# Performance work log

Measured on AMD Instinct MI355X. Metric: run time of the kernel, lower is better.

## Reference

```python
import jax, jax.numpy as jnp
import numpy as np

L_LAYERS = 2
SEQ = 2048
K_EIG = 24
D = 128
D_TGT = 64
K_U = 3
K_Y = 2
B = 8


def hankel_eigh(n, k):
    # Z[i,j] = 2 / ((i+j)^3 - (i+j)), 1-indexed; top-k eigenpairs
    s = np.arange(1, n + 1, dtype=np.float64)
    ij = s[:, None] + s[None, :]
    z = 2.0 / (ij ** 3 - ij)
    vals, vecs = np.linalg.eigh(z)
    return (jnp.asarray(vals[-k:], jnp.float32), jnp.asarray(vecs[:, -k:], jnp.float32))


def setup_inputs() -> dict:
    key = jax.random.key(0)
    ks = jax.random.split(key, 8)
    sd = 1.0 / np.sqrt(D)
    inp = {
        "x": jax.random.normal(ks[0], (B, SEQ, D), jnp.float32),
        "emb_w": jax.random.normal(ks[1], (D, D), jnp.float32) * sd,
        "emb_b": jnp.zeros((D,), jnp.float32),
        "ln_g": jnp.ones((L_LAYERS, D), jnp.float32),
        "ln_b": jnp.zeros((L_LAYERS, D), jnp.float32),
        "m_phi": jax.random.normal(ks[2], (L_LAYERS, K_EIG * D, D), jnp.float32) * sd,
        "m_u": jax.random.normal(ks[3], (L_LAYERS, D, D, K_U), jnp.float32) * sd,
        "m_y": jax.random.normal(ks[4], (L_LAYERS, D, K_Y, D), jnp.float32) * 0.01,
        "w1": jax.random.normal(ks[5], (L_LAYERS, D, 2 * D), jnp.float32) * sd,
        "b1": jnp.zeros((L_LAYERS, 2 * D), jnp.float32),
        "proj_w": jax.random.normal(ks[6], (D, D_TGT), jnp.float32) * sd,
        "proj_b": jnp.zeros((D_TGT,), jnp.float32),
    }
    ev, evec = hankel_eigh(SEQ, K_EIG)
    inp["eig_vals"] = ev
    inp["eig_vecs"] = evec
    return inp


def compute_x_tilde(x, eig_vals, eig_vecs):
    # x: [B, L, D]; causal (truncated full) convolution of each eigvec filter
    # with each input channel via FFT. Result [B, L, K, D] -> [B, L, K*D].
    n = 2 * SEQ
    V = jnp.fft.rfft(eig_vecs, n=n, axis=0)              # [nf, K]
    U = jnp.fft.rfft(x, n=n, axis=1)                     # [B, nf, D]
    conv = jnp.fft.irfft(V[None, :, :, None] * U[:, :, None, :], n=n, axis=1)[:, :SEQ]
    conv = conv * (eig_vals ** 0.25)[None, None, :, None]
    return conv.reshape(x.shape[0], SEQ, K_EIG * x.shape[-1]).astype(x.dtype)


def compute_ar_x_preds(m_u, x):
    # o[t] = sum_{i<K_U} m_u[:, :, i] @ x[t-i]  (zero for t-i < 0)
    res = jnp.einsum('bli,oi->blo', x, m_u[:, :, 0])
    for i in range(1, K_U):
        xi = jnp.pad(x, ((0, 0), (i, 0), (0, 0)))[:, :SEQ]
        res = res + jnp.einsum('bli,oi->blo', xi, m_u[:, :, i])
    return res


def compute_y_t(m_y, deltas):
    # y[t] = sum_{j<K_Y} m_y[:, j, :] @ y[t-1-j] + deltas[t]
    d = deltas.shape[-1]
    def step(carry, x):  # carry [B, K_Y, d] holds y[t-1], y[t-2], ...
        out = jnp.einsum('okd,bkd->bo', m_y, carry) + x
        carry = jnp.concatenate([out[:, None, :], carry[:, :-1]], axis=1)
        return carry, out
    init = jnp.zeros((deltas.shape[0], K_Y, d), deltas.dtype)
    _, ys = jax.lax.scan(step, init, jnp.swapaxes(deltas, 0, 1))
    return jnp.swapaxes(ys, 0, 1)


def layer_norm(x, g, b):
    mu = x.mean(-1, keepdims=True)
    var = ((x - mu) ** 2).mean(-1, keepdims=True)
    return (x - mu) / jnp.sqrt(var + 1e-5) * g + b


def reference(x, emb_w, emb_b, ln_g, ln_b, m_phi, m_u, m_y, w1, b1, proj_w, proj_b, eig_vals, eig_vecs):
    h = x @ emb_w + emb_b
    for i in range(L_LAYERS):
        z = h
        h = layer_norm(h, ln_g[i], ln_b[i])
        x_tilde = compute_x_tilde(h, eig_vals, eig_vecs)       # [B, L, K*D]
        delta = x_tilde @ m_phi[i] + compute_ar_x_preds(m_u[i], h)
        y = compute_y_t(m_y[i], delta)
        y = jax.nn.gelu(y, approximate=False)
        y = y @ w1[i] + b1[i]
        a, g = jnp.split(y, 2, axis=-1)
        h = a * jax.nn.sigmoid(g) + z                          # GLU + residual (dropout=0)
    return h @ proj_w + proj_b
```

## Files before the change

### kernel.cpp

```cpp
#include <hip/hip_runtime.h>

typedef unsigned short u16;
typedef unsigned int u32;
typedef __bf16 bf16x8 __attribute__((ext_vector_type(8)));
typedef float f32x4 __attribute__((ext_vector_type(4)));
typedef float f32x2 __attribute__((ext_vector_type(2)));
typedef u16 u16x4 __attribute__((ext_vector_type(4)));
typedef u16 u16x8 __attribute__((ext_vector_type(8)));

#define DEV static __device__ __forceinline__

static constexpr int ROWS = 8 * 2048;
static constexpr int TAPS = 24;
static constexpr int PADR = 64;
static constexpr int DROWS = 2048 + PADR;

DEV u16 f2bf(float x) {
  u32 u = __float_as_uint(x);
  u += 0x7fffu + ((u >> 16) & 1u);
  return (u16)(u >> 16);
}

DEV void gld_lds16(const u16* g, u16* l) {
  __builtin_amdgcn_global_load_lds(
      (const __attribute__((address_space(1))) u32*)g,
      (__attribute__((address_space(3))) u32*)l, 16, 0, 0);
}


__global__ void prep_toeplitz(const float* __restrict__ evec,
                              const float* __restrict__ evals,
                              u16* __restrict__ T) {
  int k = blockIdx.x / 33, ti = blockIdx.x % 33;
  float sc = powf(evals[k], 0.25f);
  u16* out = T + (size_t)blockIdx.x * 4096;
  for (int e = threadIdx.x; e < 4096; e += 256) {
    int i = e >> 6, j = e & 63;
    int tau = (ti - 1) * 64 + i - j;
    float v = (tau >= 0 && tau < 2048) ? evec[tau * 24 + k] * sc : 0.f;
    out[e] = f2bf(v);
  }
}

__global__ void transpose_w(const float* __restrict__ src, u16* __restrict__ dst,
                            int K, int N) {
  int idx = blockIdx.x * 256 + threadIdx.x;
  if (idx >= K * N) return;
  int n = idx / K, k = idx % K;
  dst[idx] = f2bf(src[(size_t)k * N + n]);
}

__global__ void prep_mphiT(const float* __restrict__ mphi,
                           const float* __restrict__ mu,
                           u16* __restrict__ dst) {
  int idx = blockIdx.x * 256 + threadIdx.x;
  if (idx >= 128 * 3456) return;
  int o = idx / 3456, c = idx % 3456;
  float v;
  if (c < 3072) {
    v = mphi[(size_t)c * 128 + o];
  } else {
    int cc = c - 3072;
    int j = cc >> 7, i = cc & 127;
    v = mu[((size_t)o * 128 + i) * 3 + j];
  }
  dst[idx] = f2bf(v);
}

__global__ void f32_to_bf16_k(const float* __restrict__ src, u16* __restrict__ dst,
                              int n4) {
  int i = blockIdx.x * 256 + threadIdx.x;
  if (i >= n4) return;
  f32x4 v = *(const f32x4*)(src + (size_t)i * 4);
  u16x4 o;
  o[0] = f2bf(v[0]); o[1] = f2bf(v[1]); o[2] = f2bf(v[2]); o[3] = f2bf(v[3]);
  *(u16x4*)(dst + (size_t)i * 4) = o;
}

__global__ __launch_bounds__(128) void hprep_kernel(const float* __restrict__ my,
                                                    u16* __restrict__ Hp) {
  const int l = blockIdx.x >> 7, j = blockIdx.x & 127;
  const int o = threadIdx.x;
  const float* M = my + (size_t)l * 32768;
  u32 mp1[64], mp2[64];
  {
    const float* r1 = M + (size_t)o * 256;
    const float* r2 = r1 + 128;
#pragma unroll
    for (int q = 0; q < 64; ++q) {
      mp1[q] = (u32)f2bf(r1[2 * q]) | ((u32)f2bf(r1[2 * q + 1]) << 16);
      mp2[q] = (u32)f2bf(r2[2 * q]) | ((u32)f2bf(r2[2 * q + 1]) << 16);
    }
  }
  __shared__ float vb[3][128];
  u16* HpL = Hp + ((size_t)l * 128 + o) * (TAPS * 128) + j;
  float v0 = (o == j) ? 1.f : 0.f;
  vb[0][o] = v0;
  vb[2][o] = 0.f;
  HpL[0] = f2bf(v0);
  __syncthreads();
  for (int tau = 1; tau < TAPS; ++tau) {
    const int a = (tau + 2) % 3;
    const int b = (tau + 1) % 3;
    const int c = tau % 3;
    const float* v1 = vb[a];
    const float* v2 = vb[b];
    float acc = 0.f;
#pragma unroll
    for (int q = 0; q < 64; ++q) {
      u32 w1 = mp1[q], w2 = mp2[q];
      float m1lo = __uint_as_float(w1 << 16);
      float m1hi = __uint_as_float(w1 & 0xffff0000u);
      float m2lo = __uint_as_float(w2 << 16);
      float m2hi = __uint_as_float(w2 & 0xffff0000u);
      acc += m1lo * v1[2 * q] + m1hi * v1[2 * q + 1];
      acc += m2lo * v2[2 * q] + m2hi * v2[2 * q + 1];
    }
    vb[c][o] = acc;
    HpL[tau * 128] = f2bf(acc);
    __syncthreads();
  }
}

__global__ void zero_pad(u16* __restrict__ dpad) {
  int i = blockIdx.x * 256 + threadIdx.x;
  int b = i >> 10, off = i & 1023;
  *(u16x8*)(dpad + (size_t)b * DROWS * 128 + off * 8) = (u16x8){0, 0, 0, 0, 0, 0, 0, 0};
}


__global__ __launch_bounds__(256) void ln_kernel(
    const float* __restrict__ h, const float* __restrict__ gam,
    const float* __restrict__ bet, u16* __restrict__ out) {
  int row = blockIdx.x * 4 + (threadIdx.x >> 6);
  int lane = threadIdx.x & 63;
  f32x2 v = *(const f32x2*)(h + (size_t)row * 128 + lane * 2);
  float s = v[0] + v[1];
#pragma unroll
  for (int o = 32; o; o >>= 1) s += __shfl_xor(s, o);
  float mu = s * (1.f / 128.f);
  float dx = v[0] - mu, dy = v[1] - mu;
  float q = dx * dx + dy * dy;
#pragma unroll
  for (int o = 32; o; o >>= 1) q += __shfl_xor(q, o);
  float rstd = rsqrtf(q * (1.f / 128.f) + 1e-5f);
  f32x2 g2 = *(const f32x2*)(gam + lane * 2);
  f32x2 b2 = *(const f32x2*)(bet + lane * 2);
  float o0 = dx * rstd * g2[0] + b2[0];
  float o1 = dy * rstd * g2[1] + b2[1];
  u32 pk = (u32)f2bf(o0) | ((u32)f2bf(o1) << 16);
  *(u32*)(out + (size_t)row * 128 + lane * 2) = pk;
}

__global__ __launch_bounds__(256) void transpose_hln(
    const u16* __restrict__ src, u16* __restrict__ dst) {
  __shared__ u16 tile[64][72];
  int blk = blockIdx.x;
  int b = blk >> 6, rem = blk & 63;
  int st = rem >> 1, dt = rem & 1;
  int r = threadIdx.x >> 2, cseg = (threadIdx.x & 3) << 4;
  const u16* s = src + ((size_t)(b * 2048 + st * 64 + r)) * 128 + dt * 64 + cseg;
  u16x8 v0 = *(const u16x8*)s;
  u16x8 v1 = *(const u16x8*)(s + 8);
#pragma unroll
  for (int i = 0; i < 8; ++i) tile[r][cseg + i] = v0[i];
#pragma unroll
  for (int i = 0; i < 8; ++i) tile[r][cseg + 8 + i] = v1[i];
  __syncthreads();
  int dr = threadIdx.x >> 2, sseg = (threadIdx.x & 3) << 4;
  u16x8 w0, w1;
#pragma unroll
  for (int i = 0; i < 8; ++i) w0[i] = tile[sseg + i][dr];
#pragma unroll
  for (int i = 0; i < 8; ++i) w1[i] = tile[sseg + 8 + i][dr];
  u16* d = dst + ((size_t)(b * 128 + dt * 64 + dr)) * 2048 + st * 64 + sseg;
  *(u16x8*)d = w0;
  *(u16x8*)(d + 8) = w1;
}

__global__ void shift_kernel(const u16* __restrict__ hln, u16* __restrict__ xtc) {
  int row = blockIdx.x;
  int t = row & 2047;
  int d = threadIdx.x;
#pragma unroll
  for (int j = 0; j < 3; ++j) {
    u16 v = (t >= j) ? hln[(size_t)(row - j) * 128 + d] : (u16)0;
    xtc[(size_t)row * 3456 + 3072 + j * 128 + d] = v;
  }
}

__global__ void glu_kernel(const float* __restrict__ y2, float* __restrict__ h,
                           u16* __restrict__ hbf, int n4) {
  int i = blockIdx.x * 256 + threadIdx.x;
  if (i >= n4) return;
  int row = i >> 5, d4 = i & 31;
  f32x4 a = *(const f32x4*)(y2 + (size_t)row * 256 + d4 * 4);
  f32x4 g = *(const f32x4*)(y2 + (size_t)row * 256 + 128 + d4 * 4);
  f32x4 hv = *(const f32x4*)(h + (size_t)i * 4);
  f32x4 hn;
  u16x4 o;
#pragma unroll
  for (int j = 0; j < 4; ++j) {
    hn[j] = a[j] * (1.f / (1.f + expf(-g[j]))) + hv[j];
    o[j] = f2bf(hn[j]);
  }
  *(f32x4*)(h + (size_t)i * 4) = hn;
  *(u16x4*)(hbf + (size_t)i * 4) = o;
}


template <int BM, int BN>
__global__ __launch_bounds__(256) void gemm_bt(
    const u16* __restrict__ A, int lda, const u16* __restrict__ BT, int ldbt,
    float* __restrict__ C, int ldc, const float* __restrict__ bias, int kBlocks,
    int accumulate, u16* __restrict__ Cbf) {
  constexpr int WROWS = (BN == 64) ? 4 : 2;
  constexpr int WCOLS = (BN == 64) ? 1 : 2;
  constexpr int WTM = BM / WROWS;
  constexpr int WTN = BN / WCOLS;
  constexpr int FM = WTM / 16;
  constexpr int FN = WTN / 16;
  __shared__ u16 As[BM * 64];
  __shared__ u16 Bs[BN * 64];
  const int tid = threadIdx.x;
  const int wid = tid >> 6, lane = tid & 63;
  const int bm = blockIdx.x, bn = blockIdx.y;
  const int wr = wid / WCOLS, wc = wid % WCOLS;
  const int r = lane & 15, hi = lane >> 4;

  f32x4 acc[FM][FN];
#pragma unroll
  for (int i = 0; i < FM; ++i)
#pragma unroll
    for (int j = 0; j < FN; ++j) acc[i][j] = (f32x4){0.f, 0.f, 0.f, 0.f};

  for (int kb = 0; kb < kBlocks; ++kb) {
    if (kb) __syncthreads();
#pragma unroll
    for (int it = 0; it < BM / 32; ++it) {
      int ci = it * 256 + tid;
      int sc = (ci & 7) ^ ((ci >> 3) & 7);
      gld_lds16(A + (size_t)(bm * BM + (ci >> 3)) * lda + kb * 64 + sc * 8,
                &As[(it * 256 + wid * 64) * 8]);
    }
#pragma unroll
    for (int it = 0; it < BN / 32; ++it) {
      int ci = it * 256 + tid;
      int sc = (ci & 7) ^ ((ci >> 3) & 7);
      gld_lds16(BT + (size_t)(bn * BN + (ci >> 3)) * ldbt + kb * 64 + sc * 8,
                &Bs[(it * 256 + wid * 64) * 8]);
    }
    __syncthreads();
#pragma unroll
    for (int ks = 0; ks < 2; ++ks) {
      const int sk = ((ks * 4 + hi) ^ (r & 7)) << 3;
      bf16x8 af[FM], bfv[FN];
#pragma unroll
      for (int fm = 0; fm < FM; ++fm)
        af[fm] = *(const bf16x8*)&As[(wr * WTM + fm * 16 + r) * 64 + sk];
#pragma unroll
      for (int fn = 0; fn < FN; ++fn)
        bfv[fn] = *(const bf16x8*)&Bs[(wc * WTN + fn * 16 + r) * 64 + sk];
#pragma unroll
      for (int fm = 0; fm < FM; ++fm)
#pragma unroll
        for (int fn = 0; fn < FN; ++fn)
          acc[fm][fn] = __builtin_amdgcn_mfma_f32_16x16x32_bf16(
              af[fm], bfv[fn], acc[fm][fn], 0, 0, 0);
    }
  }
#pragma unroll
  for (int fm = 0; fm < FM; ++fm) {
#pragma unroll
    for (int fn = 0; fn < FN; ++fn) {
      const int col = bn * BN + wc * WTN + fn * 16 + r;
      const float bv = bias ? bias[col] : 0.f;
#pragma unroll
      for (int q = 0; q < 4; ++q) {
        const int row = bm * BM + wr * WTM + fm * 16 + hi * 4 + q;
        float v = acc[fm][fn][q] + bv;
        if (C) {
          float* cp = &C[(size_t)row * ldc + col];
          if (accumulate) v += *cp;
          *cp = v;
        }
        if (Cbf) {
          int bb = row >> 11, t = row & 2047;
          Cbf[((size_t)(bb * DROWS + PADR + t)) * 128 + col] = f2bf(v);
        }
      }
    }
  }
}

__global__ __launch_bounds__(256) void gemm_conv(
    const u16* __restrict__ T, const u16* __restrict__ hlnT,
    u16* __restrict__ xtc) {
  __shared__ u16 As[128 * 64];
  __shared__ u16 Bs[128 * 64];
  const int tid = threadIdx.x;
  const int wid = tid >> 6, lane = tid & 63;
  const int tt = blockIdx.x / 192;
  const int rem = blockIdx.x % 192;
  const int kc = rem >> 3, b = rem & 7;
  const int t0 = (15 - tt) << 7;
  const int r = lane & 15, hi = lane >> 4;
  const int wr = wid >> 1, wc = wid & 1;

  f32x4 acc[4][4];
#pragma unroll
  for (int i = 0; i < 4; ++i)
#pragma unroll
    for (int j = 0; j < 4; ++j) acc[i][j] = (f32x4){0.f, 0.f, 0.f, 0.f};

  const u16* Tk = T + (size_t)kc * 33 * 4096;
  const u16* Bb = hlnT + (size_t)b * 128 * 2048;
  const int nsb = (t0 >> 6) + 2;

  for (int sb = 0; sb < nsb; ++sb) {
    const int dlt = (t0 >> 6) - sb;
    if (sb) __syncthreads();
#pragma unroll
    for (int it = 0; it < 4; ++it) {
      int ci = it * 256 + tid;
      int ti = (ci < 512) ? (dlt + 1) : (dlt + 2);
      int lc = ci & 511;
      int sc = (lc & 7) ^ ((lc >> 3) & 7);
      gld_lds16(Tk + (size_t)ti * 4096 + (lc >> 3) * 64 + sc * 8,
                &As[(it * 256 + wid * 64) * 8]);
    }
#pragma unroll
    for (int it = 0; it < 4; ++it) {
      int ci = it * 256 + tid;
      int sc = (ci & 7) ^ ((ci >> 3) & 7);
      gld_lds16(Bb + (size_t)(ci >> 3) * 2048 + sb * 64 + sc * 8,
                &Bs[(it * 256 + wid * 64) * 8]);
    }
    __syncthreads();
#pragma unroll
    for (int ks = 0; ks < 2; ++ks) {
      const int sk = ((ks * 4 + hi) ^ (r & 7)) << 3;
      bf16x8 af[4], bfv[4];
#pragma unroll
      for (int fm = 0; fm < 4; ++fm)
        af[fm] = *(const bf16x8*)&As[(wr * 64 + fm * 16 + r) * 64 + sk];
#pragma unroll
      for (int fn = 0; fn < 4; ++fn)
        bfv[fn] = *(const bf16x8*)&Bs[(wc * 64 + fn * 16 + r) * 64 + sk];
#pragma unroll
      for (int fm = 0; fm < 4; ++fm)
#pragma unroll
        for (int fn = 0; fn < 4; ++fn)
          acc[fm][fn] = __builtin_amdgcn_mfma_f32_16x16x32_bf16(
              af[fm], bfv[fn], acc[fm][fn], 0, 0, 0);
    }
  }
#pragma unroll
  for (int fm = 0; fm < 4; ++fm) {
#pragma unroll
    for (int fn = 0; fn < 4; ++fn) {
      const int col = wc * 64 + fn * 16 + r;
#pragma unroll
      for (int q = 0; q < 4; ++q) {
        const int row = t0 + wr * 64 + fm * 16 + hi * 4 + q;
        xtc[((size_t)(b * 2048 + row)) * 3456 + kc * 128 + col] = f2bf(acc[fm][fn][q]);
      }
    }
  }
}

__global__ __launch_bounds__(256) void gemm_yconv(
    const u16* __restrict__ dpad, const u16* __restrict__ Hp,
    u16* __restrict__ ybf) {
  __shared__ u16 As[64 * 64];
  __shared__ u16 Bs[64 * 64];
  const int tid = threadIdx.x;
  const int wid = tid >> 6, lane = tid & 63;
  const int bm = blockIdx.x, bn = blockIdx.y;
  const int b = bm >> 5, t0 = (bm & 31) << 6;
  const int r = lane & 15, hi = lane >> 4;

  f32x4 acc[4];
#pragma unroll
  for (int j = 0; j < 4; ++j) acc[j] = (f32x4){0.f, 0.f, 0.f, 0.f};

  const u16* Ab = dpad + (size_t)b * DROWS * 128;
  for (int kb = 0; kb < TAPS * 2; ++kb) {
    const int tap = kb >> 1, i0 = (kb & 1) << 6;
    const u16* Ap = Ab + (size_t)(PADR + t0 - tap) * 128 + i0;
    if (kb) __syncthreads();
#pragma unroll
    for (int it = 0; it < 2; ++it) {
      int ci = it * 256 + tid;
      int sc = (ci & 7) ^ ((ci >> 3) & 7);
      gld_lds16(Ap + (size_t)(ci >> 3) * 128 + sc * 8,
                &As[(it * 256 + wid * 64) * 8]);
    }
#pragma unroll
    for (int it = 0; it < 2; ++it) {
      int ci = it * 256 + tid;
      int sc = (ci & 7) ^ ((ci >> 3) & 7);
      gld_lds16(Hp + (size_t)(bn * 64 + (ci >> 3)) * (TAPS * 128) + kb * 64 + sc * 8,
                &Bs[(it * 256 + wid * 64) * 8]);
    }
    __syncthreads();
#pragma unroll
    for (int ks = 0; ks < 2; ++ks) {
      const int sk = ((ks * 4 + hi) ^ (r & 7)) << 3;
      bf16x8 af = *(const bf16x8*)&As[(wid * 16 + r) * 64 + sk];
      bf16x8 bfv[4];
#pragma unroll
      for (int fn = 0; fn < 4; ++fn)
        bfv[fn] = *(const bf16x8*)&Bs[(fn * 16 + r) * 64 + sk];
#pragma unroll
      for (int fn = 0; fn < 4; ++fn)
        acc[fn] = __builtin_amdgcn_mfma_f32_16x16x32_bf16(af, bfv[fn], acc[fn], 0, 0, 0);
    }
  }
#pragma unroll
  for (int fn = 0; fn < 4; ++fn) {
    const int col = bn * 64 + fn * 16 + r;
#pragma unroll
    for (int q = 0; q < 4; ++q) {
      const int row = t0 + wid * 16 + hi * 4 + q;
      float v = acc[fn][q];
      float gl = 0.5f * v * (1.f + erff(v * 0.70710678118654752f));
      ybf[((size_t)(b * 2048 + row)) * 128 + col] = f2bf(gl);
    }
  }
}


extern "C" void kernel_launch(void* const* d_in, const int* in_sizes, int n_in,
                              void* d_out, int out_size, void* d_ws, size_t ws_size,
                              hipStream_t stream) {
  (void)in_sizes; (void)n_in; (void)out_size; (void)ws_size;
  const float* x = (const float*)d_in[0];
  const float* emb_w = (const float*)d_in[1];
  const float* emb_b = (const float*)d_in[2];
  const float* ln_g = (const float*)d_in[3];
  const float* ln_b = (const float*)d_in[4];
  const float* m_phi = (const float*)d_in[5];
  const float* m_u = (const float*)d_in[6];
  const float* m_y = (const float*)d_in[7];
  const float* w1 = (const float*)d_in[8];
  const float* b1 = (const float*)d_in[9];
  const float* proj_w = (const float*)d_in[10];
  const float* proj_b = (const float*)d_in[11];
  const float* evals = (const float*)d_in[12];
  const float* evec = (const float*)d_in[13];
  float* out = (float*)d_out;

  char* p = (char*)d_ws;
  auto carve = [&](size_t bytes) {
    char* r = p;
    p += (bytes + 255) & ~(size_t)255;
    return r;
  };
  u16* Tbuf = (u16*)carve((size_t)24 * 33 * 4096 * 2);
  u16* embT = (u16*)carve(128 * 128 * 2);
  u16* w1T = (u16*)carve((size_t)2 * 256 * 128 * 2);
  u16* projT = (u16*)carve(64 * 128 * 2);
  u16* mphiT = (u16*)carve((size_t)2 * 128 * 3456 * 2);
  u16* Hp = (u16*)carve((size_t)2 * 128 * TAPS * 128 * 2);
  u16* xbf = (u16*)carve((size_t)ROWS * 128 * 2);
  float* h = (float*)carve((size_t)ROWS * 128 * 4);
  u16* hbf = (u16*)carve((size_t)ROWS * 128 * 2);
  u16* hlnbf = (u16*)carve((size_t)ROWS * 128 * 2);
  u16* hlnT = (u16*)carve((size_t)ROWS * 128 * 2);
  u16* xtc = (u16*)carve((size_t)ROWS * 3456 * 2);
  u16* dpad = (u16*)carve((size_t)8 * DROWS * 128 * 2);
  u16* ybf = (u16*)carve((size_t)ROWS * 128 * 2);
  float* y2 = (float*)carve((size_t)ROWS * 256 * 4);

  prep_toeplitz<<<dim3(24 * 33), dim3(256), 0, stream>>>(evec, evals, Tbuf);
  hprep_kernel<<<dim3(256), dim3(128), 0, stream>>>(m_y, Hp);
  zero_pad<<<dim3(32), dim3(256), 0, stream>>>(dpad);
  transpose_w<<<dim3(64), dim3(256), 0, stream>>>(emb_w, embT, 128, 128);
  transpose_w<<<dim3(128), dim3(256), 0, stream>>>(w1, w1T, 128, 256);
  transpose_w<<<dim3(128), dim3(256), 0, stream>>>(w1 + 128 * 256, w1T + 256 * 128, 128, 256);
  transpose_w<<<dim3(32), dim3(256), 0, stream>>>(proj_w, projT, 128, 64);
  prep_mphiT<<<dim3(1728), dim3(256), 0, stream>>>(m_phi, m_u, mphiT);
  prep_mphiT<<<dim3(1728), dim3(256), 0, stream>>>(
      m_phi + (size_t)3072 * 128, m_u + (size_t)128 * 128 * 3, mphiT + (size_t)128 * 3456);
  f32_to_bf16_k<<<dim3(2048), dim3(256), 0, stream>>>(x, xbf, ROWS * 128 / 4);

  gemm_bt<64, 128><<<dim3(256, 1), dim3(256), 0, stream>>>(
      xbf, 128, embT, 128, h, 128, emb_b, 2, 0, nullptr);

  for (int l = 0; l < 2; ++l) {
    ln_kernel<<<dim3(4096), dim3(256), 0, stream>>>(h, ln_g + l * 128, ln_b + l * 128, hlnbf);
    transpose_hln<<<dim3(512), dim3(256), 0, stream>>>(hlnbf, hlnT);
    shift_kernel<<<dim3(16384), dim3(128), 0, stream>>>(hlnbf, xtc);
    const u16* mT = mphiT + (size_t)l * 128 * 3456;
    gemm_conv<<<dim3(3072), dim3(256), 0, stream>>>(Tbuf, hlnT, xtc);
    gemm_bt<64, 64><<<dim3(256, 2), dim3(256), 0, stream>>>(
        xtc, 3456, mT, 3456, nullptr, 0, nullptr, 54, 0, dpad);
    gemm_yconv<<<dim3(256, 2), dim3(256), 0, stream>>>(
        dpad, Hp + (size_t)l * 128 * TAPS * 128, ybf);
    gemm_bt<64, 128><<<dim3(256, 2), dim3(256), 0, stream>>>(
        ybf, 128, w1T + (size_t)l * 256 * 128, 128, y2, 256, b1 + l * 256, 2, 0, nullptr);
    glu_kernel<<<dim3(2048), dim3(256), 0, stream>>>(y2, h, hbf, ROWS * 32);
  }

  gemm_bt<128, 64><<<dim3(128, 1), dim3(256), 0, stream>>>(
      hbf, 128, projT, 128, out, 64, proj_b, 2, 0, nullptr);
}
```

Before: 507.2 us.

## Fuse spectral conv with m_phi projection, LN with transpose, and w1 GEMM with GLU

The separate Toeplitz conv GEMM that wrote a large bf16 x_tilde buffer, followed by a big K=3456 projection GEMM, is replaced by a fused kernel. Each block convolves four eigen-filters, stages each result in LDS and immediately multiplies it by the matching m_phi slice. Partial sums go to seven fp32 slots (six filter groups plus the AR shift GEMM) and a reduce kernel sums them into the padded delta buffer. LayerNorm and the transpose are merged into one kernel, and the w1 GEMM is fused with the GLU and residual, so the y2 round trip disappears. The cost is extra fp32 partial-buffer traffic and a reduction pass, re-rounding of the conv output to bf16 per filter, and lower occupancy from the larger LDS footprint.

```diff
diff --git a/kernel.cpp b/kernel.cpp
--- a/kernel.cpp
+++ b/kernel.cpp
@@ -14,6 +14,7 @@
 static constexpr int TAPS = 24;
 static constexpr int PADR = 64;
 static constexpr int DROWS = 2048 + PADR;
+static constexpr size_t PSLOT = (size_t)ROWS * 128;
 
 DEV u16 f2bf(float x) {
   u32 u = __float_as_uint(x);
@@ -129,91 +130,78 @@
 }
 
 
-__global__ __launch_bounds__(256) void ln_kernel(
+__global__ __launch_bounds__(256) void ln_tr_kernel(
     const float* __restrict__ h, const float* __restrict__ gam,
-    const float* __restrict__ bet, u16* __restrict__ out) {
-  int row = blockIdx.x * 4 + (threadIdx.x >> 6);
-  int lane = threadIdx.x & 63;
-  f32x2 v = *(const f32x2*)(h + (size_t)row * 128 + lane * 2);
-  float s = v[0] + v[1];
-#pragma unroll
-  for (int o = 32; o; o >>= 1) s += __shfl_xor(s, o);
-  float mu = s * (1.f / 128.f);
-  float dx = v[0] - mu, dy = v[1] - mu;
-  float q = dx * dx + dy * dy;
-#pragma unroll
-  for (int o = 32; o; o >>= 1) q += __shfl_xor(q, o);
-  float rstd = rsqrtf(q * (1.f / 128.f) + 1e-5f);
+    const float* __restrict__ bet, u16* __restrict__ hlnbf,
+    u16* __restrict__ hlnT) {
+  __shared__ u16 tile[64][136];
+  const int b = blockIdx.x >> 5, st = blockIdx.x & 31;
+  const int wrow = threadIdx.x >> 6;
+  const int lane = threadIdx.x & 63;
   f32x2 g2 = *(const f32x2*)(gam + lane * 2);
   f32x2 b2 = *(const f32x2*)(bet + lane * 2);
-  float o0 = dx * rstd * g2[0] + b2[0];
-  float o1 = dy * rstd * g2[1] + b2[1];
-  u32 pk = (u32)f2bf(o0) | ((u32)f2bf(o1) << 16);
-  *(u32*)(out + (size_t)row * 128 + lane * 2) = pk;
-}
-
-__global__ __launch_bounds__(256) void transpose_hln(
-    const u16* __restrict__ src, u16* __restrict__ dst) {
-  __shared__ u16 tile[64][72];
-  int blk = blockIdx.x;
-  int b = blk >> 6, rem = blk & 63;
-  int st = rem >> 1, dt = rem & 1;
-  int r = threadIdx.x >> 2, cseg = (threadIdx.x & 3) << 4;
-  const u16* s = src + ((size_t)(b * 2048 + st * 64 + r)) * 128 + dt * 64 + cseg;
-  u16x8 v0 = *(const u16x8*)s;
-  u16x8 v1 = *(const u16x8*)(s + 8);
-#pragma unroll
-  for (int i = 0; i < 8; ++i) tile[r][cseg + i] = v0[i];
-#pragma unroll
-  for (int i = 0; i < 8; ++i) tile[r][cseg + 8 + i] = v1[i];
+#pragma unroll 4
+  for (int it = 0; it < 16; ++it) {
+    int lr = it * 4 + wrow;
+    size_t row = (size_t)b * 2048 + st * 64 + lr;
+    f32x2 v = *(const f32x2*)(h + row * 128 + lane * 2);
+    float s = v[0] + v[1];
+#pragma unroll
+    for (int o = 32; o; o >>= 1) s += __shfl_xor(s, o);
+    float mu = s * (1.f / 128.f);
+    float dx = v[0] - mu, dy = v[1] - mu;
+    float q = dx * dx + dy * dy;
+#pragma unroll
+    for (int o = 32; o; o >>= 1) q += __shfl_xor(q, o);
+    float rstd = rsqrtf(q * (1.f / 128.f) + 1e-5f);
+    float o0 = dx * rstd * g2[0] + b2[0];
+    float o1 = dy * rstd * g2[1] + b2[1];
+    u32 pk = (u32)f2bf(o0) | ((u32)f2bf(o1) << 16);
+    *(u32*)(hlnbf + row * 128 + lane * 2) = pk;
+    *(u32*)&tile[lr][lane * 2] = pk;
+  }
   __syncthreads();
-  int dr = threadIdx.x >> 2, sseg = (threadIdx.x & 3) << 4;
-  u16x8 w0, w1;
-#pragma unroll
-  for (int i = 0; i < 8; ++i) w0[i] = tile[sseg + i][dr];
-#pragma unroll
-  for (int i = 0; i < 8; ++i) w1[i] = tile[sseg + 8 + i][dr];
-  u16* d = dst + ((size_t)(b * 128 + dt * 64 + dr)) * 2048 + st * 64 + sseg;
-  *(u16x8*)d = w0;
-  *(u16x8*)(d + 8) = w1;
-}
-
-__global__ void shift_kernel(const u16* __restrict__ hln, u16* __restrict__ xtc) {
+  const int d = threadIdx.x >> 1;
+  const int half = threadIdx.x & 1;
+#pragma unroll
+  for (int i = 0; i < 4; ++i) {
+    int sg = half * 4 + i;
+    u16x8 w;
+#pragma unroll
+    for (int j = 0; j < 8; ++j) w[j] = tile[sg * 8 + j][d];
+    *(u16x8*)(hlnT + ((size_t)b * 128 + d) * 2048 + st * 64 + sg * 8) = w;
+  }
+}
+
+__global__ void shift_kernel(const u16* __restrict__ hln, u16* __restrict__ out) {
   int row = blockIdx.x;
   int t = row & 2047;
   int d = threadIdx.x;
 #pragma unroll
   for (int j = 0; j < 3; ++j) {
     u16 v = (t >= j) ? hln[(size_t)(row - j) * 128 + d] : (u16)0;
-    xtc[(size_t)row * 3456 + 3072 + j * 128 + d] = v;
-  }
-}
-
-__global__ void glu_kernel(const float* __restrict__ y2, float* __restrict__ h,
-                           u16* __restrict__ hbf, int n4) {
+    out[(size_t)row * 384 + j * 128 + d] = v;
+  }
+}
+
+__global__ void reduce_kernel(const float* __restrict__ parts,
+                              u16* __restrict__ dpad) {
   int i = blockIdx.x * 256 + threadIdx.x;
-  if (i >= n4) return;
+  f32x4 s = *(const f32x4*)(parts + (size_t)i * 4);
+#pragma unroll
+  for (int g = 1; g < 7; ++g) s += *(const f32x4*)(parts + g * PSLOT + (size_t)i * 4);
   int row = i >> 5, d4 = i & 31;
-  f32x4 a = *(const f32x4*)(y2 + (size_t)row * 256 + d4 * 4);
-  f32x4 g = *(const f32x4*)(y2 + (size_t)row * 256 + 128 + d4 * 4);
-  f32x4 hv = *(const f32x4*)(h + (size_t)i * 4);
-  f32x4 hn;
+  int b = row >> 11, t = row & 2047;
   u16x4 o;
-#pragma unroll
-  for (int j = 0; j < 4; ++j) {
-    hn[j] = a[j] * (1.f / (1.f + expf(-g[j]))) + hv[j];
-    o[j] = f2bf(hn[j]);
-  }
-  *(f32x4*)(h + (size_t)i * 4) = hn;
-  *(u16x4*)(hbf + (size_t)i * 4) = o;
+  o[0] = f2bf(s[0]); o[1] = f2bf(s[1]); o[2] = f2bf(s[2]); o[3] = f2bf(s[3]);
+  *(u16x4*)(dpad + ((size_t)(b * DROWS + PADR + t)) * 128 + d4 * 4) = o;
 }
 
 
 template <int BM, int BN>
 __global__ __launch_bounds__(256) void gemm_bt(
     const u16* __restrict__ A, int lda, const u16* __restrict__ BT, int ldbt,
-    float* __restrict__ C, int ldc, const float* __restrict__ bias, int kBlocks,
-    int accumulate, u16* __restrict__ Cbf) {
+    float* __restrict__ C, int ldc, const float* __restrict__ bias, int kBlocks) {
   constexpr int WROWS = (BN == 64) ? 4 : 2;
   constexpr int WCOLS = (BN == 64) ? 1 : 2;
   constexpr int WTM = BM / WROWS;
@@ -278,95 +266,137 @@
 #pragma unroll
       for (int q = 0; q < 4; ++q) {
         const int row = bm * BM + wr * WTM + fm * 16 + hi * 4 + q;
-        float v = acc[fm][fn][q] + bv;
-        if (C) {
-          float* cp = &C[(size_t)row * ldc + col];
-          if (accumulate) v += *cp;
-          *cp = v;
-        }
-        if (Cbf) {
-          int bb = row >> 11, t = row & 2047;
-          Cbf[((size_t)(bb * DROWS + PADR + t)) * 128 + col] = f2bf(v);
-        }
-      }
-    }
-  }
-}
-
-__global__ __launch_bounds__(256) void gemm_conv(
+        C[(size_t)row * ldc + col] = acc[fm][fn][q] + bv;
+      }
+    }
+  }
+}
+
+__global__ __launch_bounds__(256) void gemm_convd(
     const u16* __restrict__ T, const u16* __restrict__ hlnT,
-    u16* __restrict__ xtc) {
-  __shared__ u16 As[128 * 64];
+    const u16* __restrict__ mphiT, float* __restrict__ parts) {
+  __shared__ u16 As[64 * 64];
   __shared__ u16 Bs[128 * 64];
+  __shared__ u16 Ps[64 * 128];
   const int tid = threadIdx.x;
   const int wid = tid >> 6, lane = tid & 63;
-  const int tt = blockIdx.x / 192;
-  const int rem = blockIdx.x % 192;
-  const int kc = rem >> 3, b = rem & 7;
-  const int t0 = (15 - tt) << 7;
+  const int tt = blockIdx.x / 48;
+  const int rem = blockIdx.x % 48;
+  const int g = rem >> 3, b = rem & 7;
+  const int t0 = (31 - tt) << 6;
+  const int nsb = (t0 >> 6) + 1;
+  const int wr = wid >> 1, wc = wid & 1;
   const int r = lane & 15, hi = lane >> 4;
-  const int wr = wid >> 1, wc = wid & 1;
-
-  f32x4 acc[4][4];
-#pragma unroll
-  for (int i = 0; i < 4; ++i)
-#pragma unroll
-    for (int j = 0; j < 4; ++j) acc[i][j] = (f32x4){0.f, 0.f, 0.f, 0.f};
-
-  const u16* Tk = T + (size_t)kc * 33 * 4096;
+
+  f32x4 accd[2][4];
+#pragma unroll
+  for (int i = 0; i < 2; ++i)
+#pragma unroll
+    for (int j = 0; j < 4; ++j) accd[i][j] = (f32x4){0.f, 0.f, 0.f, 0.f};
+
   const u16* Bb = hlnT + (size_t)b * 128 * 2048;
-  const int nsb = (t0 >> 6) + 2;
-
-  for (int sb = 0; sb < nsb; ++sb) {
-    const int dlt = (t0 >> 6) - sb;
-    if (sb) __syncthreads();
-#pragma unroll
-    for (int it = 0; it < 4; ++it) {
-      int ci = it * 256 + tid;
-      int ti = (ci < 512) ? (dlt + 1) : (dlt + 2);
-      int lc = ci & 511;
-      int sc = (lc & 7) ^ ((lc >> 3) & 7);
-      gld_lds16(Tk + (size_t)ti * 4096 + (lc >> 3) * 64 + sc * 8,
-                &As[(it * 256 + wid * 64) * 8]);
-    }
-#pragma unroll
-    for (int it = 0; it < 4; ++it) {
-      int ci = it * 256 + tid;
-      int sc = (ci & 7) ^ ((ci >> 3) & 7);
-      gld_lds16(Bb + (size_t)(ci >> 3) * 2048 + sb * 64 + sc * 8,
-                &Bs[(it * 256 + wid * 64) * 8]);
-    }
-    __syncthreads();
-#pragma unroll
-    for (int ks = 0; ks < 2; ++ks) {
-      const int sk = ((ks * 4 + hi) ^ (r & 7)) << 3;
-      bf16x8 af[4], bfv[4];
-#pragma unroll
-      for (int fm = 0; fm < 4; ++fm)
-        af[fm] = *(const bf16x8*)&As[(wr * 64 + fm * 16 + r) * 64 + sk];
-#pragma unroll
-      for (int fn = 0; fn < 4; ++fn)
-        bfv[fn] = *(const bf16x8*)&Bs[(wc * 64 + fn * 16 + r) * 64 + sk];
-#pragma unroll
-      for (int fm = 0; fm < 4; ++fm)
+
+  for (int f = 0; f < 4; ++f) {
+    const int k = g * 4 + f;
+    const u16* Tk = T + (size_t)k * 33 * 4096;
+    f32x4 accc[2][4];
+#pragma unroll
+    for (int i = 0; i < 2; ++i)
+#pragma unroll
+      for (int j = 0; j < 4; ++j) accc[i][j] = (f32x4){0.f, 0.f, 0.f, 0.f};
+
+    for (int sb = 0; sb < nsb; ++sb) {
+      const int ti = (t0 >> 6) - sb + 1;
+      __syncthreads();
+#pragma unroll
+      for (int it = 0; it < 2; ++it) {
+        int ci = it * 256 + tid;
+        int sc = (ci & 7) ^ ((ci >> 3) & 7);
+        gld_lds16(Tk + (size_t)ti * 4096 + (ci >> 3) * 64 + sc * 8,
+                  &As[(it * 256 + wid * 64) * 8]);
+      }
+#pragma unroll
+      for (int it = 0; it < 4; ++it) {
+        int ci = it * 256 + tid;
+        int sc = (ci & 7) ^ ((ci >> 3) & 7);
+        gld_lds16(Bb + (size_t)(ci >> 3) * 2048 + sb * 64 + sc * 8,
+                  &Bs[(it * 256 + wid * 64) * 8]);
+      }
+      __syncthreads();
+#pragma unroll
+      for (int ks = 0; ks < 2; ++ks) {
+        const int sk = ((ks * 4 + hi) ^ (r & 7)) << 3;
+        bf16x8 af[2], bfv[4];
+#pragma unroll
+        for (int fm = 0; fm < 2; ++fm)
+          af[fm] = *(const bf16x8*)&As[(wr * 32 + fm * 16 + r) * 64 + sk];
 #pragma unroll
         for (int fn = 0; fn < 4; ++fn)
-          acc[fm][fn] = __builtin_amdgcn_mfma_f32_16x16x32_bf16(
-              af[fm], bfv[fn], acc[fm][fn], 0, 0, 0);
-    }
-  }
-#pragma unroll
-  for (int fm = 0; fm < 4; ++fm) {
+          bfv[fn] = *(const bf16x8*)&Bs[(wc * 64 + fn * 16 + r) * 64 + sk];
+#pragma unroll
+        for (int fm = 0; fm < 2; ++fm)
+#pragma unroll
+          for (int fn = 0; fn < 4; ++fn)
+            accc[fm][fn] = __builtin_amdgcn_mfma_f32_16x16x32_bf16(
+                af[fm], bfv[fn], accc[fm][fn], 0, 0, 0);
+      }
+    }
+#pragma unroll
+    for (int fm = 0; fm < 2; ++fm)
+#pragma unroll
+      for (int fn = 0; fn < 4; ++fn) {
+        const int pcol = wc * 64 + fn * 16 + r;
+        const int c = pcol >> 3;
+#pragma unroll
+        for (int q = 0; q < 4; ++q) {
+          const int prow = wr * 32 + fm * 16 + hi * 4 + q;
+          Ps[prow * 128 + ((c ^ (prow & 7)) << 3) + (pcol & 7)] =
+              f2bf(accc[fm][fn][q]);
+        }
+      }
+#pragma unroll
+    for (int dh = 0; dh < 2; ++dh) {
+      __syncthreads();
+#pragma unroll
+      for (int it = 0; it < 4; ++it) {
+        int ci = it * 256 + tid;
+        int sc = (ci & 7) ^ ((ci >> 3) & 7);
+        gld_lds16(mphiT + (size_t)(ci >> 3) * 3456 + k * 128 + dh * 64 + sc * 8,
+                  &Bs[(it * 256 + wid * 64) * 8]);
+      }
+      __syncthreads();
+#pragma unroll
+      for (int ks = 0; ks < 2; ++ks) {
+        const int sk2 = ((dh * 8 + ks * 4 + hi) ^ (r & 7)) << 3;
+        const int sk = ((ks * 4 + hi) ^ (r & 7)) << 3;
+        bf16x8 pa[2], bfv[4];
+#pragma unroll
+        for (int fm = 0; fm < 2; ++fm)
+          pa[fm] = *(const bf16x8*)&Ps[(wr * 32 + fm * 16 + r) * 128 + sk2];
+#pragma unroll
+        for (int fn = 0; fn < 4; ++fn)
+          bfv[fn] = *(const bf16x8*)&Bs[(wc * 64 + fn * 16 + r) * 64 + sk];
+#pragma unroll
+        for (int fm = 0; fm < 2; ++fm)
+#pragma unroll
+          for (int fn = 0; fn < 4; ++fn)
+            accd[fm][fn] = __builtin_amdgcn_mfma_f32_16x16x32_bf16(
+                pa[fm], bfv[fn], accd[fm][fn], 0, 0, 0);
+      }
+    }
+  }
+  float* P = parts + g * PSLOT + ((size_t)b * 2048) * 128;
+#pragma unroll
+  for (int fm = 0; fm < 2; ++fm)
 #pragma unroll
     for (int fn = 0; fn < 4; ++fn) {
       const int col = wc * 64 + fn * 16 + r;
 #pragma unroll
       for (int q = 0; q < 4; ++q) {
-        const int row = t0 + wr * 64 + fm * 16 + hi * 4 + q;
-        xtc[((size_t)(b * 2048 + row)) * 3456 + kc * 128 + col] = f2bf(acc[fm][fn][q]);
-      }
-    }
-  }
+        const int row = t0 + wr * 32 + fm * 16 + hi * 4 + q;
+        P[(size_t)row * 128 + col] = accd[fm][fn][q];
+      }
+    }
 }
 
 __global__ __launch_bounds__(256) void gemm_yconv(
@@ -427,6 +457,97 @@
       float gl = 0.5f * v * (1.f + erff(v * 0.70710678118654752f));
       ybf[((size_t)(b * 2048 + row)) * 128 + col] = f2bf(gl);
     }
+  }
+}
+
+__global__ __launch_bounds__(256) void gemm_w1glu(
+    const u16* __restrict__ ybf, const u16* __restrict__ w1T,
+    const float* __restrict__ b1, float* __restrict__ h,
+    u16* __restrict__ hbf) {
+  __shared__ u16 As[64 * 64];
+  __shared__ u16 Bs[256 * 64];
+  __shared__ float sg[64][128];
+  const int tid = threadIdx.x;
+  const int wid = tid >> 6, lane = tid & 63;
+  const int bm = blockIdx.x;
+  const int wr = wid >> 1, wc = wid & 1;
+  const int r = lane & 15, hi = lane >> 4;
+
+  f32x4 acc[2][8];
+#pragma unroll
+  for (int i = 0; i < 2; ++i)
+#pragma unroll
+    for (int j = 0; j < 8; ++j) acc[i][j] = (f32x4){0.f, 0.f, 0.f, 0.f};
+
+  for (int kb = 0; kb < 2; ++kb) {
+    if (kb) __syncthreads();
+#pragma unroll
+    for (int it = 0; it < 2; ++it) {
+      int ci = it * 256 + tid;
+      int sc = (ci & 7) ^ ((ci >> 3) & 7);
+      gld_lds16(ybf + (size_t)(bm * 64 + (ci >> 3)) * 128 + kb * 64 + sc * 8,
+                &As[(it * 256 + wid * 64) * 8]);
+    }
+#pragma unroll
+    for (int it = 0; it < 8; ++it) {
+      int ci = it * 256 + tid;
+      int sc = (ci & 7) ^ ((ci >> 3) & 7);
+      gld_lds16(w1T + (size_t)(ci >> 3) * 128 + kb * 64 + sc * 8,
+                &Bs[(it * 256 + wid * 64) * 8]);
+    }
+    __syncthreads();
+#pragma unroll
+    for (int ks = 0; ks < 2; ++ks) {
+      const int sk = ((ks * 4 + hi) ^ (r & 7)) << 3;
+      bf16x8 af[2], bfv[8];
+#pragma unroll
+      for (int fm = 0; fm < 2; ++fm)
+        af[fm] = *(const bf16x8*)&As[(wr * 32 + fm * 16 + r) * 64 + sk];
+#pragma unroll
+      for (int fn = 0; fn < 8; ++fn)
+        bfv[fn] = *(const bf16x8*)&Bs[(wc * 128 + fn * 16 + r) * 64 + sk];
+#pragma unroll
+      for (int fm = 0; fm < 2; ++fm)
+#pragma unroll
+        for (int fn = 0; fn < 8; ++fn)
+          acc[fm][fn] = __builtin_amdgcn_mfma_f32_16x16x32_bf16(
+              af[fm], bfv[fn], acc[fm][fn], 0, 0, 0);
+    }
+  }
+  __syncthreads();
+  if (wc == 1) {
+#pragma unroll
+    for (int fm = 0; fm < 2; ++fm)
+#pragma unroll
+      for (int fn = 0; fn < 8; ++fn) {
+        const int colg = fn * 16 + r;
+        const float bv = b1[128 + colg];
+#pragma unroll
+        for (int q = 0; q < 4; ++q) {
+          const int rl = wr * 32 + fm * 16 + hi * 4 + q;
+          float v = acc[fm][fn][q] + bv;
+          sg[rl][colg] = 1.f / (1.f + expf(-v));
+        }
+      }
+  }
+  __syncthreads();
+  if (wc == 0) {
+#pragma unroll
+    for (int fm = 0; fm < 2; ++fm)
+#pragma unroll
+      for (int fn = 0; fn < 8; ++fn) {
+        const int col = fn * 16 + r;
+        const float bv = b1[col];
+#pragma unroll
+        for (int q = 0; q < 4; ++q) {
+          const int rl = wr * 32 + fm * 16 + hi * 4 + q;
+          const size_t row = (size_t)bm * 64 + rl;
+          float a = acc[fm][fn][q] + bv;
+          float hn = a * sg[rl][col] + h[row * 128 + col];
+          h[row * 128 + col] = hn;
+          hbf[row * 128 + col] = f2bf(hn);
+        }
+      }
   }
 }
 
@@ -468,10 +589,10 @@
   u16* hbf = (u16*)carve((size_t)ROWS * 128 * 2);
   u16* hlnbf = (u16*)carve((size_t)ROWS * 128 * 2);
   u16* hlnT = (u16*)carve((size_t)ROWS * 128 * 2);
-  u16* xtc = (u16*)carve((size_t)ROWS * 3456 * 2);
+  u16* shifts = (u16*)carve((size_t)ROWS * 384 * 2);
+  float* parts = (float*)carve((size_t)7 * PSLOT * 4);
   u16* dpad = (u16*)carve((size_t)8 * DROWS * 128 * 2);
   u16* ybf = (u16*)carve((size_t)ROWS * 128 * 2);
-  float* y2 = (float*)carve((size_t)ROWS * 256 * 4);
 
   prep_toeplitz<<<dim3(24 * 33), dim3(256), 0, stream>>>(evec, evals, Tbuf);
   hprep_kernel<<<dim3(256), dim3(128), 0, stream>>>(m_y, Hp);
@@ -486,23 +607,23 @@
   f32_to_bf16_k<<<dim3(2048), dim3(256), 0, stream>>>(x, xbf, ROWS * 128 / 4);
 
   gemm_bt<64, 128><<<dim3(256, 1), dim3(256), 0, stream>>>(
-      xbf, 128, embT, 128, h, 128, emb_b, 2, 0, nullptr);
+      xbf, 128, embT, 128, h, 128, emb_b, 2);
 
   for (int l = 0; l < 2; ++l) {
-    ln_kernel<<<dim3(4096), dim3(256), 0, stream>>>(h, ln_g + l * 128, ln_b + l * 128, hlnbf);
-    transpose_hln<<<dim3(512), dim3(256), 0, stream>>>(hlnbf, hlnT);
-    shift_kernel<<<dim3(16384), dim3(128), 0, stream>>>(hlnbf, xtc);
     const u16* mT = mphiT + (size_t)l * 128 * 3456;
-    gemm_conv<<<dim3(3072), dim3(256), 0, stream>>>(Tbuf, hlnT, xtc);
-    gemm_bt<64, 64><<<dim3(256, 2), dim3(256), 0, stream>>>(
-        xtc, 3456, mT, 3456, nullptr, 0, nullptr, 54, 0, dpad);
+    ln_tr_kernel<<<dim3(256), dim3(256), 0, stream>>>(
+        h, ln_g + l * 128, ln_b + l * 128, hlnbf, hlnT);
+    shift_kernel<<<dim3(16384), dim3(128), 0, stream>>>(hlnbf, shifts);
+    gemm_convd<<<dim3(1536), dim3(256), 0, stream>>>(Tbuf, hlnT, mT, parts);
+    gemm_bt<64, 128><<<dim3(256, 1), dim3(256), 0, stream>>>(
+        shifts, 384, mT + 3072, 3456, parts + 6 * PSLOT, 128, nullptr, 6);
+    reduce_kernel<<<dim3(2048), dim3(256), 0, stream>>>(parts, dpad);
     gemm_yconv<<<dim3(256, 2), dim3(256), 0, stream>>>(
         dpad, Hp + (size_t)l * 128 * TAPS * 128, ybf);
-    gemm_bt<64, 128><<<dim3(256, 2), dim3(256), 0, stream>>>(
-        ybf, 128, w1T + (size_t)l * 256 * 128, 128, y2, 256, b1 + l * 256, 2, 0, nullptr);
-    glu_kernel<<<dim3(2048), dim3(256), 0, stream>>>(y2, h, hbf, ROWS * 32);
+    gemm_w1glu<<<dim3(256), dim3(256), 0, stream>>>(
+        ybf, w1T + (size_t)l * 256 * 128, b1 + l * 256, h, hbf);
   }
 
   gemm_bt<128, 64><<<dim3(128, 1), dim3(256), 0, stream>>>(
-      hbf, 128, projT, 128, out, 64, proj_b, 2, 0, nullptr);
-}
+      hbf, 128, projT, 128, out, 64, proj_b, 2);
+}
```

After: 630.7 us. 1.24x slower.
